# Performance work log

Hardware: AMD Instinct MI355X
Metric: run time of the kernel (lower is better)

## Reference

```python
import jax, jax.numpy as jnp
import numpy as np

NU, NI, ED, H = 30000, 10000, 64, 4
D = ED * H            # fusion_dim = 256
N = NU + NI           # total graph nodes
E = 100000            # edges
B = 8192              # scored (user, wine) pairs
NST, SD = 4, 64       # side tokens / side token dim
NEG = -1e30


def setup_inputs():
    key = jax.random.key(0)
    ks = iter(jax.random.split(key, 64))

    def w(*shape):
        return jax.random.normal(next(ks), shape, jnp.float32) * 0.05

    return {
        "user": jax.random.randint(next(ks), (B,), 0, NU),
        "wine": jax.random.randint(next(ks), (B,), 0, NI),
        "edge_index": jax.random.randint(next(ks), (2, E), 0, N),
        "keep_edge": jax.random.uniform(next(ks), (E,)) > 0.2,   # edge_dropout keep mask
        "node_mask": jax.random.uniform(next(ks), (N,)) < 0.2,   # mask-autoencoding mask
        "user_emb": w(NU, ED),
        "wine_emb": w(NI, ED),
        "up_w": w(ED, D), "up_b": w(D),
        "wp_w": w(ED, D), "wp_b": w(D),
        "sf_proj_w": w(SD, D), "sf_proj_b": w(D),
        "sf_q_w": w(D, D), "sf_q_b": w(D),
        "sf_k_w": w(D, D), "sf_k_b": w(D),
        "sf_v_w": w(D, D), "sf_v_b": w(D),
        "sf_o_w": w(D, D), "sf_o_b": w(D),
        "sf_fc_w": w(2 * D, D), "sf_fc_b": w(D),
        "g_w": w(D, D), "g_b": w(D),
        "t_q_w": w(D, H * D), "t_q_b": w(H * D),
        "t_k_w": w(D, H * D), "t_k_b": w(H * D),
        "t_v_w": w(D, H * D), "t_v_b": w(H * D),
        "t_skip_w": w(D, D), "t_skip_b": w(D),
        "fc_w": w(2 * D, 1), "fc_b": w(1),
        "ae_w": w(D, D), "ae_b": w(D),
        "ep_w": w(2 * D, 1), "ep_b": w(1),
        "wine_side_features": jax.random.normal(next(ks), (NI, NST, SD), jnp.float32),
    }


def _forward(user, wine, edge_index, keep_edge, node_mask,
             user_emb, wine_emb, up_w, up_b, wp_w, wp_b,
             sf_proj_w, sf_proj_b, sf_q_w, sf_q_b, sf_k_w, sf_k_b,
             sf_v_w, sf_v_b, sf_o_w, sf_o_b, sf_fc_w, sf_fc_b,
             g_w, g_b, t_q_w, t_q_b, t_k_w, t_k_b, t_v_w, t_v_b,
             t_skip_w, t_skip_b, fc_w, fc_b, ae_w, ae_b, ep_w, ep_b,
             wine_side_features):
    u_proj = user_emb @ up_w + up_b                       # [NU, D]
    w_proj = wine_emb @ wp_w + wp_b                       # [NI, D]

    # WineSideFusion: single-head attention of wine embedding over side tokens
    side = wine_side_features @ sf_proj_w + sf_proj_b     # [NI, T, D]
    q = w_proj @ sf_q_w + sf_q_b                          # [NI, D]
    k = side @ sf_k_w + sf_k_b                            # [NI, T, D]
    v = side @ sf_v_w + sf_v_b
    attn = jax.nn.softmax(jnp.einsum('nd,ntd->nt', q, k) / jnp.sqrt(jnp.float32(D)), axis=-1)
    ao = jnp.einsum('nt,ntd->nd', attn, v) @ sf_o_w + sf_o_b
    fused = jnp.concatenate([w_proj, ao], axis=1) @ sf_fc_w + sf_fc_b

    x = jnp.concatenate([u_proj, fused], axis=0)          # [N, D]
    src, dst = edge_index[0], edge_index[1]
    ew = keep_edge.astype(x.dtype)                        # edge dropout as 0/1 weights

    # GCNConv (add self loops, symmetric norm)
    deg = jax.ops.segment_sum(ew, dst, num_segments=N) + 1.0
    dinv = jax.lax.rsqrt(deg)
    norm = dinv[src] * dinv[dst] * ew                     # [E]
    xw = x @ g_w                                          # [N, D]
    agg = jax.ops.segment_sum(xw[src] * norm[:, None], dst, num_segments=N)
    x = agg + xw * (dinv * dinv)[:, None] + g_b

    # TransformerConv(heads=H, concat=False): mean over heads + skip
    qh = (x @ t_q_w + t_q_b).reshape(N, H, D)
    kh = (x @ t_k_w + t_k_b).reshape(N, H, D)
    vh = (x @ t_v_w + t_v_b).reshape(N, H, D)
    logits = jnp.einsum('ehd,ehd->eh', qh[dst], kh[src]) / jnp.sqrt(jnp.float32(D))
    logits = jnp.where(keep_edge[:, None], logits, NEG)
    m = jax.ops.segment_max(logits, dst, num_segments=N)  # [N, H]
    m = jnp.where(m < NEG / 2, 0.0, m)                    # guard empty segments
    e = jnp.exp(logits - m[dst]) * ew[:, None]            # [E, H]
    den = jax.ops.segment_sum(e, dst, num_segments=N)     # [N, H]
    num = jax.ops.segment_sum(e[:, :, None] * vh[src], dst, num_segments=N)  # [N, H, D]
    attn_out = num / jnp.maximum(den, 1e-16)[:, :, None]
    x = attn_out.mean(axis=1) + x @ t_skip_w + t_skip_b   # [N, D]

    # Masked autoencoding: masked rows are zeroed, then autoencoded -> recon = bias
    maskf = node_mask.astype(x.dtype)
    recon = ae_b                                          # 0 @ ae_w + ae_b
    diff = recon[None, :] - x                             # [N, D]
    recon_loss = jnp.sum(maskf[:, None] * diff * diff) / (jnp.sum(maskf) * D)

    u_out = x[user]                                       # [B, D]
    w_out = x[wine + NU]                                  # [B, D]
    pair = jnp.concatenate([u_out, w_out], axis=1)        # [B, 2D]

    edge_score = jax.nn.sigmoid(pair @ ep_w + ep_b)       # [B, 1]
    edge_pred_loss = jnp.mean((edge_score - 1.0) ** 2)

    score = jax.nn.sigmoid((pair @ fc_w + fc_b).squeeze(-1)) * 4.0 + 1.0  # [B]
    return score, recon_loss, edge_pred_loss


def reference(user, wine, edge_index, keep_edge, node_mask,
              user_emb, wine_emb, up_w, up_b, wp_w, wp_b,
              sf_proj_w, sf_proj_b, sf_q_w, sf_q_b, sf_k_w, sf_k_b,
              sf_v_w, sf_v_b, sf_o_w, sf_o_b, sf_fc_w, sf_fc_b,
              g_w, g_b, t_q_w, t_q_b, t_k_w, t_k_b, t_v_w, t_v_b,
              t_skip_w, t_skip_b, fc_w, fc_b, ae_w, ae_b, ep_w, ep_b,
              wine_side_features):
    return _forward(user, wine, edge_index, keep_edge, node_mask,
                    user_emb, wine_emb, up_w, up_b, wp_w, wp_b,
                    sf_proj_w, sf_proj_b, sf_q_w, sf_q_b, sf_k_w, sf_k_b,
                    sf_v_w, sf_v_b, sf_o_w, sf_o_b, sf_fc_w, sf_fc_b,
                    g_w, g_b, t_q_w, t_q_b, t_k_w, t_k_b, t_v_w, t_v_b,
                    t_skip_w, t_skip_b, fc_w, fc_b, ae_w, ae_b, ep_w, ep_b,
                    wine_side_features)
```

## Files before the change

### kernel.cpp

```cpp
#include <hip/hip_runtime.h>
#include <stdint.h>

typedef unsigned short u16;
typedef unsigned char u8;
typedef __attribute__((ext_vector_type(8))) short bf16x8;
typedef __attribute__((ext_vector_type(4))) float f32x4;

#define NU_C 30000
#define NI_C 10000
#define N_C  40000
#define E_C  100000
#define B_C  8192

static __device__ __forceinline__ float bf2f(u16 u) {
    union { unsigned int i; float f; } c; c.i = ((unsigned int)u) << 16; return c.f;
}
static __device__ __forceinline__ u16 f2bf(float f) {
    union { float f; unsigned int i; } c; c.f = f;
    return (u16)((c.i + 0x7FFFu + ((c.i >> 16) & 1u)) >> 16);
}
static __device__ __forceinline__ float wave_sum(float v) {
#pragma unroll
    for (int off = 32; off > 0; off >>= 1) v += __shfl_xor(v, off);
    return v;
}
static __device__ __forceinline__ float group_sum16(float v) {
#pragma unroll
    for (int off = 8; off > 0; off >>= 1) v += __shfl_xor(v, off);
    return v;
}
static __device__ __forceinline__ float dot16(const bf16x8 a0, const bf16x8 a1,
                                              const bf16x8 b0, const bf16x8 b1) {
    float p = 0.f;
#pragma unroll
    for (int j = 0; j < 8; ++j) p = fmaf(bf2f((u16)a0[j]), bf2f((u16)b0[j]), p);
#pragma unroll
    for (int j = 0; j < 8; ++j) p = fmaf(bf2f((u16)a1[j]), bf2f((u16)b1[j]), p);
    return p;
}

__global__ void zero_kernel(unsigned int* p, int n) {
    int i = blockIdx.x * 256 + threadIdx.x;
    if (i < n) p[i] = 0u;
}
__global__ void fillval_kernel(float* p, int n, float v) {
    int i = blockIdx.x * 256 + threadIdx.x;
    if (i < n) p[i] = v;
}

__global__ void detect_kernel(const unsigned int* a, int n, int* flag) {
    int i = blockIdx.x * 256 + threadIdx.x;
    if (i >= n) return;
    unsigned int v = a[i];
    int f = 0;
    if (v > 1u) f |= 1;
    if (v != 0u && v != 0x3F800000u) f |= 2;
    if (f) atomicOr(flag, f);
}
__global__ void conv_masks_kernel(const void* keep_raw, const void* nm_raw,
                                  u8* km, u8* nm, int E, int N, const int* flag)
{
    int i = blockIdx.x * 256 + threadIdx.x;
    const int f = *flag;
    if (i < E) {
        u8 r;
        if ((f & 1) == 0)      r = ((const int*)keep_raw)[i] != 0;
        else if ((f & 2) == 0) r = ((const float*)keep_raw)[i] != 0.f;
        else                   r = ((const u8*)keep_raw)[i] != 0;
        km[i] = r;
    }
    int j = i - E;
    if (j >= 0 && j < N) {
        u8 r;
        if ((f & 1) == 0)      r = ((const int*)nm_raw)[j] != 0;
        else if ((f & 2) == 0) r = ((const float*)nm_raw)[j] != 0.f;
        else                   r = ((const u8*)nm_raw)[j] != 0;
        nm[j] = r;
    }
}

__global__ void conv3_kernel(const float* __restrict__ a, int na4,
                             const float* __restrict__ b, int nb4,
                             const float* __restrict__ c, int nc4,
                             u16* __restrict__ oa, u16* __restrict__ ob, u16* __restrict__ oc)
{
    int tot = na4 + nb4 + nc4;
    for (int i = blockIdx.x * 256 + threadIdx.x; i < tot; i += gridDim.x * 256) {
        const float* s; u16* o; int j = i;
        if (j < na4) { s = a; o = oa; }
        else if ((j -= na4) < nb4) { s = b; o = ob; }
        else { j -= nb4; s = c; o = oc; }
        float4 v = *(const float4*)&s[(size_t)j * 4];
        ushort4 r;
        r.x = f2bf(v.x); r.y = f2bf(v.y); r.z = f2bf(v.z); r.w = f2bf(v.w);
        *(ushort4*)&o[(size_t)j * 4] = r;
    }
}

#define WT_ELEMS 1359872
__device__ const int wd_prefix[23] = {0,16384,32768,49152,114688,180224,245760,311296,442368,
    507904,573440,638976,704512,770048,835584,901120,966656,1032192,1097728,1163264,1228800,
    1294336,1359872};
__device__ const u8  wd_src[22]  = {0,1,2,3,4,5,6,7,8,9,10,11,12,10,11,12,10,11,12,10,11,12};
__device__ const short wd_ldw[22]= {256,256,256,256,256,256,256,256,256,256,
    1024,1024,1024,1024,1024,1024,1024,1024,1024,1024,1024,1024};
__device__ const short wd_coff[22]={0,0,0,0,0,0,0,0,0,0, 0,0,0, 256,256,256, 512,512,512, 768,768,768};
__device__ const short wd_kmask[22]={63,63,63,255,255,255,255,511,255,255,
    255,255,255,255,255,255,255,255,255,255,255,255};
__device__ const u8  wd_ksh[22] = {6,6,6,8,8,8,8,9,8,8, 8,8,8,8,8,8,8,8,8,8,8,8};

__global__ __launch_bounds__(256)
void wtrans_kernel(const float* w0, const float* w1, const float* w2, const float* w3,
                   const float* w4, const float* w5, const float* w6, const float* w7,
                   const float* w8, const float* w9, const float* w10, const float* w11,
                   const float* w12, u16* __restrict__ WT)
{
    int idx = blockIdx.x * 256 + threadIdx.x;
    if (idx >= WT_ELEMS) return;
    int d = 0;
    while (wd_prefix[d + 1] <= idx) ++d;
    const int local = idx - wd_prefix[d];
    const int k = local & wd_kmask[d];
    const int n = local >> wd_ksh[d];
    const float* s;
    switch (wd_src[d]) {
        case 0: s = w0; break; case 1: s = w1; break; case 2: s = w2; break;
        case 3: s = w3; break; case 4: s = w4; break; case 5: s = w5; break;
        case 6: s = w6; break; case 7: s = w7; break; case 8: s = w8; break;
        case 9: s = w9; break; case 10: s = w10; break; case 11: s = w11; break;
        default: s = w12; break;
    }
    WT[idx] = f2bf(s[(size_t)k * wd_ldw[d] + wd_coff[d] + n]);
}

__global__ void prep_bias_kernel(const float* sfk_b, const float* sfv_b,
                                 const float* tq_b, const float* tk_b, const float* tv_b,
                                 float* kvb, float* qkvb)
{
    int i = blockIdx.x * 256 + threadIdx.x;
    if (i < 512) kvb[i] = i < 256 ? sfk_b[i] : sfv_b[i - 256];
    if (i < 3072) {
        int h = i / 768, j = i - h * 768;
        qkvb[i] = j < 256 ? tq_b[h * 256 + j]
                : (j < 512 ? tk_b[h * 256 + j - 256] : tv_b[h * 256 + j - 512]);
    }
}

template <typename OT>
__global__ __launch_bounds__(512)
void mgemm_kernel(const u16* __restrict__ A, int lda,
                  const u16* __restrict__ WT,
                  const float* __restrict__ bias,
                  OT* __restrict__ C, int ldc,
                  int M, int N, int K)
{
    __shared__ __align__(16) u16 As[256][72];
    __shared__ __align__(16) u16 Bs[128][72];
    const int t = threadIdx.x;
    const int wid = t >> 6, lane = t & 63;
    const int wr = wid >> 1, wc = wid & 1;
    const int lr = lane & 15, lg = lane >> 4;
    const int gx = gridDim.x;
    const int nwg = gx * gridDim.y;
    const int orig = blockIdx.y * gx + blockIdx.x;
    const int q8 = nwg >> 3, r8 = nwg & 7;
    const int xcd = orig & 7, oidx = orig >> 3;
    const int swzb = (xcd < r8 ? xcd * (q8 + 1) : r8 * (q8 + 1) + (xcd - r8) * q8) + oidx;
    const int row0 = (swzb / gx) * 256, col0 = (swzb % gx) * 128;
    const int sra = t >> 1, sha = (t & 1) * 32;
    const int srb = t >> 2, shb = (t & 3) * 16;
    const bool avalid = (row0 + sra) < M;
    const u16* aptr = &A[(size_t)min(row0 + sra, M - 1) * lda];
    const u16* bptr = &WT[(size_t)(col0 + srb) * K];
    const bf16x8 z = {0, 0, 0, 0, 0, 0, 0, 0};
    f32x4 acc[4][4] = {};
    bf16x8 ra[4], rb[2];

    auto gload = [&](int k0) {
#pragma unroll
        for (int j = 0; j < 4; ++j)
            ra[j] = avalid ? *(const bf16x8*)&aptr[k0 + sha + j * 8] : z;
#pragma unroll
        for (int j = 0; j < 2; ++j)
            rb[j] = *(const bf16x8*)&bptr[k0 + shb + j * 8];
    };
    auto swrite = [&]() {
#pragma unroll
        for (int j = 0; j < 4; ++j)
            *(bf16x8*)&As[sra][sha + j * 8] = ra[j];
#pragma unroll
        for (int j = 0; j < 2; ++j)
            *(bf16x8*)&Bs[srb][shb + j * 8] = rb[j];
    };
    auto compute = [&]() {
#pragma unroll
        for (int kk = 0; kk < 2; ++kk) {
            bf16x8 af[4], bfr[4];
#pragma unroll
            for (int m = 0; m < 4; ++m)
                af[m] = *(const bf16x8*)&As[wr * 64 + m * 16 + lr][kk * 32 + lg * 8];
#pragma unroll
            for (int n = 0; n < 4; ++n)
                bfr[n] = *(const bf16x8*)&Bs[wc * 64 + n * 16 + lr][kk * 32 + lg * 8];
#pragma unroll
            for (int m = 0; m < 4; ++m)
#pragma unroll
                for (int n = 0; n < 4; ++n)
                    acc[m][n] = __builtin_amdgcn_mfma_f32_16x16x32_bf16(af[m], bfr[n], acc[m][n], 0, 0, 0);
        }
    };

    gload(0);
    swrite();
    __syncthreads();
    for (int k0 = 64; k0 < K; k0 += 64) {
        gload(k0);
        compute();
        __syncthreads();
        swrite();
        __syncthreads();
    }
    compute();

#pragma unroll
    for (int m = 0; m < 4; ++m) {
#pragma unroll
        for (int r = 0; r < 4; ++r) {
            int row = row0 + wr * 64 + m * 16 + lg * 4 + r;
            if (row >= M) continue;
#pragma unroll
            for (int n = 0; n < 4; ++n) {
                int col = col0 + wc * 64 + n * 16 + lr;
                float v = acc[m][n][r];
                if (bias) v += bias[col];
                if constexpr (sizeof(OT) == 4) C[(size_t)row * ldc + col] = v;
                else C[(size_t)row * ldc + col] = f2bf(v);
            }
        }
    }
}

__global__ __launch_bounds__(256)
void side_attn_kernel(const u16* __restrict__ q, const u16* __restrict__ kv,
                      u16* __restrict__ ao, int NI)
{
    const int wid = threadIdx.x >> 6, lane = threadIdx.x & 63;
    const int n = blockIdx.x * 4 + wid;
    if (n >= NI) return;
    const ushort4 qu = *(const ushort4*)&q[(size_t)n * 256 + lane * 4];
    const float q0 = bf2f(qu.x), q1 = bf2f(qu.y), q2 = bf2f(qu.z), q3 = bf2f(qu.w);
    float logit[4];
#pragma unroll
    for (int tk = 0; tk < 4; ++tk) {
        const ushort4 ku = *(const ushort4*)&kv[((size_t)n * 4 + tk) * 512 + lane * 4];
        float p = q0 * bf2f(ku.x) + q1 * bf2f(ku.y) + q2 * bf2f(ku.z) + q3 * bf2f(ku.w);
        logit[tk] = wave_sum(p) * (1.f / 16.f);
    }
    float mx = fmaxf(fmaxf(logit[0], logit[1]), fmaxf(logit[2], logit[3]));
    float e[4], den = 0.f;
#pragma unroll
    for (int tk = 0; tk < 4; ++tk) { e[tk] = __expf(logit[tk] - mx); den += e[tk]; }
    const float inv = 1.f / den;
    float o0 = 0.f, o1 = 0.f, o2 = 0.f, o3 = 0.f;
#pragma unroll
    for (int tk = 0; tk < 4; ++tk) {
        const ushort4 vu = *(const ushort4*)&kv[((size_t)n * 4 + tk) * 512 + 256 + lane * 4];
        const float w = e[tk] * inv;
        o0 = fmaf(w, bf2f(vu.x), o0); o1 = fmaf(w, bf2f(vu.y), o1);
        o2 = fmaf(w, bf2f(vu.z), o2); o3 = fmaf(w, bf2f(vu.w), o3);
    }
    ushort4 o;
    o.x = f2bf(o0); o.y = f2bf(o1); o.z = f2bf(o2); o.w = f2bf(o3);
    *(ushort4*)&ao[(size_t)n * 256 + lane * 4] = o;
}

__global__ void count_kernel(const int* __restrict__ dst, const u8* __restrict__ keep,
                             int* __restrict__ cnt, float* __restrict__ degw, int E)
{
    int e = blockIdx.x * 256 + threadIdx.x;
    if (e >= E) return;
    int d = dst[e];
    atomicAdd(&cnt[d], 1);
    if (keep[e]) atomicAdd(&degw[d], 1.f);
}

__global__ void dinv_kernel(const float* __restrict__ degw, float* __restrict__ dinv, int N)
{
    int n = blockIdx.x * 256 + threadIdx.x;
    if (n < N) dinv[n] = rsqrtf(degw[n] + 1.f);
}

__global__ __launch_bounds__(1024)
void scan_kernel(const int* __restrict__ cnt, int* __restrict__ rs, int n)
{
    __shared__ int wsum[17];
    __shared__ int s_run;
    const int t = threadIdx.x, lane = t & 63, wid = t >> 6;
    if (t == 0) s_run = 0;
    __syncthreads();
    for (int base = 0; base < n; base += 1024) {
        int i = base + t;
        int v = (i < n) ? cnt[i] : 0;
        int x = v;
#pragma unroll
        for (int off = 1; off < 64; off <<= 1) {
            int y = __shfl_up(x, off);
            if (lane >= off) x += y;
        }
        if (lane == 63) wsum[wid] = x;
        __syncthreads();
        if (t == 0) {
            int a = 0;
            for (int j = 0; j < 16; ++j) { int tmp = wsum[j]; wsum[j] = a; a += tmp; }
            wsum[16] = a;
        }
        __syncthreads();
        if (i < n) rs[i] = s_run + wsum[wid] + x - v;
        __syncthreads();
        if (t == 0) s_run += wsum[16];
        __syncthreads();
    }
    if (t == 0) rs[n] = s_run;
}

__global__ void fill_kernel(const int* __restrict__ dst, const int* __restrict__ rs,
                            int* __restrict__ cursor, int* __restrict__ eid, int E)
{
    int e = blockIdx.x * 256 + threadIdx.x;
    if (e >= E) return;
    int d = dst[e];
    int p = atomicAdd(&cursor[d], 1);
    eid[rs[d] + p] = e;
}

__global__ void sort_kernel(const int* __restrict__ rs, int* __restrict__ eid, int N)
{
    int n = blockIdx.x * 256 + threadIdx.x;
    if (n >= N) return;
    const int b = rs[n], len = rs[n + 1] - b;
    for (int i = 1; i < len; ++i) {
        int key = eid[b + i];
        int j = i - 1;
        while (j >= 0 && eid[b + j] > key) { eid[b + j + 1] = eid[b + j]; --j; }
        eid[b + j + 1] = key;
    }
}

__global__ void edge_prep_kernel(const int* __restrict__ eid, const int* __restrict__ src,
                                 const int* __restrict__ dst, const u8* __restrict__ keep,
                                 const float* __restrict__ dinv,
                                 int* __restrict__ ssrc, float* __restrict__ wnorm, int E)
{
    int i = blockIdx.x * 256 + threadIdx.x;
    if (i >= E) return;
    const int e = eid[i];
    const int s = src[e];
    const u8 k = keep[e];
    ssrc[i] = s * 2 + (int)k;
    wnorm[i] = k ? dinv[s] * dinv[dst[e]] : 0.f;
}

__global__ __launch_bounds__(256)
void gcn_kernel(const u16* __restrict__ xw, const int* __restrict__ ssrc,
                const float* __restrict__ wnorm, const int* __restrict__ rs,
                const float* __restrict__ dinv, const float* __restrict__ gb,
                u16* __restrict__ xout, int N)
{
    const int wid = threadIdx.x >> 6, lane = threadIdx.x & 63;
    const int n = blockIdx.x * 4 + wid;
    if (n >= N) return;
    const float di = dinv[n];
    const float dii = di * di;
    const ushort4 own = *(const ushort4*)&xw[(size_t)n * 256 + lane * 4];
    float a0 = bf2f(own.x) * dii, a1 = bf2f(own.y) * dii;
    float a2 = bf2f(own.z) * dii, a3 = bf2f(own.w) * dii;
    const int e0 = rs[n], e1 = rs[n + 1];
    int i = e0;
    for (; i + 1 < e1; i += 2) {
        const float wa = wnorm[i], wb = wnorm[i + 1];
        const int sa = ssrc[i] >> 1, sb = ssrc[i + 1] >> 1;
        const ushort4 ra = *(const ushort4*)&xw[(size_t)sa * 256 + lane * 4];
        const ushort4 rb = *(const ushort4*)&xw[(size_t)sb * 256 + lane * 4];
        a0 = fmaf(bf2f(rb.x), wb, fmaf(bf2f(ra.x), wa, a0));
        a1 = fmaf(bf2f(rb.y), wb, fmaf(bf2f(ra.y), wa, a1));
        a2 = fmaf(bf2f(rb.z), wb, fmaf(bf2f(ra.z), wa, a2));
        a3 = fmaf(bf2f(rb.w), wb, fmaf(bf2f(ra.w), wa, a3));
    }
    if (i < e1) {
        const float wa = wnorm[i];
        const int sa = ssrc[i] >> 1;
        const ushort4 r = *(const ushort4*)&xw[(size_t)sa * 256 + lane * 4];
        a0 = fmaf(bf2f(r.x), wa, a0); a1 = fmaf(bf2f(r.y), wa, a1);
        a2 = fmaf(bf2f(r.z), wa, a2); a3 = fmaf(bf2f(r.w), wa, a3);
    }
    const float4 g = *(const float4*)&gb[lane * 4];
    ushort4 o;
    o.x = f2bf(a0 + g.x); o.y = f2bf(a1 + g.y);
    o.z = f2bf(a2 + g.z); o.w = f2bf(a3 + g.w);
    *(ushort4*)&xout[(size_t)n * 256 + lane * 4] = o;
}

__global__ __launch_bounds__(256)
void tconv_all_kernel(const u16* __restrict__ qkv, const int* __restrict__ ssrc,
                      const int* __restrict__ rs, float* __restrict__ xacc, int N)
{
    const int wid = threadIdx.x >> 6, lane = threadIdx.x & 63;
    const int g = lane >> 4, s = lane & 15;
    const int n = blockIdx.x * 16 + wid * 4 + g;
    if (n >= N) return;
    const int e0 = rs[n], e1 = rs[n + 1];
    float fin[16] = {};
    for (int h = 0; h < 4; ++h) {
        const size_t qb0 = (size_t)n * 3072 + h * 768;
        const bf16x8 qa = *(const bf16x8*)&qkv[qb0 + s * 16];
        const bf16x8 qb = *(const bf16x8*)&qkv[qb0 + s * 16 + 8];
        float m = -1e30f, den = 0.f;
        float ac[16] = {};
        int i = e0;
        for (; i + 1 < e1; i += 2) {
            const int va = ssrc[i], vb = ssrc[i + 1];
            const size_t sa = (size_t)(va >> 1) * 3072 + h * 768;
            const size_t sb = (size_t)(vb >> 1) * 3072 + h * 768;
            const float ewa = (float)(va & 1), ewb = (float)(vb & 1);
            const bf16x8 ka0 = *(const bf16x8*)&qkv[sa + 256 + s * 16];
            const bf16x8 ka1 = *(const bf16x8*)&qkv[sa + 256 + s * 16 + 8];
            const bf16x8 kb0 = *(const bf16x8*)&qkv[sb + 256 + s * 16];
            const bf16x8 kb1 = *(const bf16x8*)&qkv[sb + 256 + s * 16 + 8];
            const bf16x8 xa0 = *(const bf16x8*)&qkv[sa + 512 + s * 16];
            const bf16x8 xa1 = *(const bf16x8*)&qkv[sa + 512 + s * 16 + 8];
            const bf16x8 xb0 = *(const bf16x8*)&qkv[sb + 512 + s * 16];
            const bf16x8 xb1 = *(const bf16x8*)&qkv[sb + 512 + s * 16 + 8];
            float pa = group_sum16(dot16(qa, qb, ka0, ka1)) * (1.f / 16.f);
            float pb = group_sum16(dot16(qa, qb, kb0, kb1)) * (1.f / 16.f);
            {
                const float mn = fmaxf(m, pa);
                const float sc = __expf(m - mn);
                const float w = __expf(pa - mn) * ewa;
                den = den * sc + w;
#pragma unroll
                for (int j = 0; j < 8; ++j) ac[j] = fmaf(w, bf2f((u16)xa0[j]), ac[j] * sc);
#pragma unroll
                for (int j = 0; j < 8; ++j) ac[8 + j] = fmaf(w, bf2f((u16)xa1[j]), ac[8 + j] * sc);
                m = mn;
            }
            {
                const float mn = fmaxf(m, pb);
                const float sc = __expf(m - mn);
                const float w = __expf(pb - mn) * ewb;
                den = den * sc + w;
#pragma unroll
                for (int j = 0; j < 8; ++j) ac[j] = fmaf(w, bf2f((u16)xb0[j]), ac[j] * sc);
#pragma unroll
                for (int j = 0; j < 8; ++j) ac[8 + j] = fmaf(w, bf2f((u16)xb1[j]), ac[8 + j] * sc);
                m = mn;
            }
        }
        if (i < e1) {
            const int va = ssrc[i];
            const size_t sa = (size_t)(va >> 1) * 3072 + h * 768;
            const float ewa = (float)(va & 1);
            const bf16x8 ka0 = *(const bf16x8*)&qkv[sa + 256 + s * 16];
            const bf16x8 ka1 = *(const bf16x8*)&qkv[sa + 256 + s * 16 + 8];
            const bf16x8 xa0 = *(const bf16x8*)&qkv[sa + 512 + s * 16];
            const bf16x8 xa1 = *(const bf16x8*)&qkv[sa + 512 + s * 16 + 8];
            float pa = group_sum16(dot16(qa, qb, ka0, ka1)) * (1.f / 16.f);
            const float mn = fmaxf(m, pa);
            const float sc = __expf(m - mn);
            const float w = __expf(pa - mn) * ewa;
            den = den * sc + w;
#pragma unroll
            for (int j = 0; j < 8; ++j) ac[j] = fmaf(w, bf2f((u16)xa0[j]), ac[j] * sc);
#pragma unroll
            for (int j = 0; j < 8; ++j) ac[8 + j] = fmaf(w, bf2f((u16)xa1[j]), ac[8 + j] * sc);
        }
        const float inv = 0.25f / fmaxf(den, 1e-16f);
#pragma unroll
        for (int j = 0; j < 16; ++j) fin[j] += ac[j] * inv;
    }
    float4* p4 = (float4*)&xacc[(size_t)n * 256 + s * 16];
#pragma unroll
    for (int q = 0; q < 4; ++q) {
        float4 cur = p4[q];
        cur.x += fin[q * 4 + 0]; cur.y += fin[q * 4 + 1];
        cur.z += fin[q * 4 + 2]; cur.w += fin[q * 4 + 3];
        p4[q] = cur;
    }
}

__global__ __launch_bounds__(256)
void tconv_head_kernel(const u16* __restrict__ qkv, const int* __restrict__ ssrc,
                       const int* __restrict__ rs, float* __restrict__ xacc, int N)
{
    const int wid = threadIdx.x >> 6, lane = threadIdx.x & 63;
    const int g = lane >> 4, s = lane & 15;
    const int n = blockIdx.x * 16 + wid * 4 + g;
    if (n >= N) return;
    const bf16x8 qa = *(const bf16x8*)&qkv[(size_t)n * 768 + s * 16];
    const bf16x8 qb = *(const bf16x8*)&qkv[(size_t)n * 768 + s * 16 + 8];
    const int e0 = rs[n], e1 = rs[n + 1];
    float m = -1e30f, den = 0.f;
    float ac[16] = {};
    int i = e0;
    for (; i + 1 < e1; i += 2) {
        const int va = ssrc[i], vb = ssrc[i + 1];
        const size_t sa = (size_t)(va >> 1) * 768, sb = (size_t)(vb >> 1) * 768;
        const float ewa = (float)(va & 1), ewb = (float)(vb & 1);
        const bf16x8 ka0 = *(const bf16x8*)&qkv[sa + 256 + s * 16];
        const bf16x8 ka1 = *(const bf16x8*)&qkv[sa + 256 + s * 16 + 8];
        const bf16x8 kb0 = *(const bf16x8*)&qkv[sb + 256 + s * 16];
        const bf16x8 kb1 = *(const bf16x8*)&qkv[sb + 256 + s * 16 + 8];
        const bf16x8 xa0 = *(const bf16x8*)&qkv[sa + 512 + s * 16];
        const bf16x8 xa1 = *(const bf16x8*)&qkv[sa + 512 + s * 16 + 8];
        const bf16x8 xb0 = *(const bf16x8*)&qkv[sb + 512 + s * 16];
        const bf16x8 xb1 = *(const bf16x8*)&qkv[sb + 512 + s * 16 + 8];
        float pa = group_sum16(dot16(qa, qb, ka0, ka1)) * (1.f / 16.f);
        float pb = group_sum16(dot16(qa, qb, kb0, kb1)) * (1.f / 16.f);
        {
            const float mn = fmaxf(m, pa);
            const float sc = __expf(m - mn);
            const float w = __expf(pa - mn) * ewa;
            den = den * sc + w;
#pragma unroll
            for (int j = 0; j < 8; ++j) ac[j] = fmaf(w, bf2f((u16)xa0[j]), ac[j] * sc);
#pragma unroll
            for (int j = 0; j < 8; ++j) ac[8 + j] = fmaf(w, bf2f((u16)xa1[j]), ac[8 + j] * sc);
            m = mn;
        }
        {
            const float mn = fmaxf(m, pb);
            const float sc = __expf(m - mn);
            const float w = __expf(pb - mn) * ewb;
            den = den * sc + w;
#pragma unroll
            for (int j = 0; j < 8; ++j) ac[j] = fmaf(w, bf2f((u16)xb0[j]), ac[j] * sc);
#pragma unroll
            for (int j = 0; j < 8; ++j) ac[8 + j] = fmaf(w, bf2f((u16)xb1[j]), ac[8 + j] * sc);
            m = mn;
        }
    }
    if (i < e1) {
        const int va = ssrc[i];
        const size_t sa = (size_t)(va >> 1) * 768;
        const float ewa = (float)(va & 1);
        const bf16x8 ka0 = *(const bf16x8*)&qkv[sa + 256 + s * 16];
        const bf16x8 ka1 = *(const bf16x8*)&qkv[sa + 256 + s * 16 + 8];
        const bf16x8 xa0 = *(const bf16x8*)&qkv[sa + 512 + s * 16];
        const bf16x8 xa1 = *(const bf16x8*)&qkv[sa + 512 + s * 16 + 8];
        float pa = group_sum16(dot16(qa, qb, ka0, ka1)) * (1.f / 16.f);
        const float mn = fmaxf(m, pa);
        const float sc = __expf(m - mn);
        const float w = __expf(pa - mn) * ewa;
        den = den * sc + w;
#pragma unroll
        for (int j = 0; j < 8; ++j) ac[j] = fmaf(w, bf2f((u16)xa0[j]), ac[j] * sc);
#pragma unroll
        for (int j = 0; j < 8; ++j) ac[8 + j] = fmaf(w, bf2f((u16)xa1[j]), ac[8 + j] * sc);
    }
    const float inv = 0.25f / fmaxf(den, 1e-16f);
    float4* p4 = (float4*)&xacc[(size_t)n * 256 + s * 16];
#pragma unroll
    for (int q = 0; q < 4; ++q) {
        float4 cur = p4[q];
        cur.x += ac[q * 4 + 0] * inv; cur.y += ac[q * 4 + 1] * inv;
        cur.z += ac[q * 4 + 2] * inv; cur.w += ac[q * 4 + 3] * inv;
        p4[q] = cur;
    }
}

__global__ __launch_bounds__(256)
void recon_kernel(const float* __restrict__ x, const u8* __restrict__ mask,
                  const float* __restrict__ aeb,
                  float* __restrict__ rblkS, float* __restrict__ rblkC, int N)
{
    const int total = N * 256;
    float s = 0.f, c = 0.f;
    for (int idx = blockIdx.x * 256 + threadIdx.x; idx < total; idx += gridDim.x * 256) {
        const int n = idx >> 8, d = idx & 255;
        if (mask[n]) {
            const float diff = aeb[d] - x[idx];
            s = fmaf(diff, diff, s);
            if (d == 0) c += 1.f;
        }
    }
    s = wave_sum(s); c = wave_sum(c);
    __shared__ float ss[4], cc[4];
    const int lane = threadIdx.x & 63, wid = threadIdx.x >> 6;
    if (lane == 0) { ss[wid] = s; cc[wid] = c; }
    __syncthreads();
    if (threadIdx.x == 0) {
        rblkS[blockIdx.x] = ss[0] + ss[1] + ss[2] + ss[3];
        rblkC[blockIdx.x] = cc[0] + cc[1] + cc[2] + cc[3];
    }
}

__global__ __launch_bounds__(256)
void score_kernel(const float* __restrict__ x, const int* __restrict__ user,
                  const int* __restrict__ wine,
                  const float* __restrict__ epw, const float* __restrict__ epb,
                  const float* __restrict__ fcw, const float* __restrict__ fcb,
                  float* __restrict__ out, float* __restrict__ sblk, int B)
{
    __shared__ float sep[4];
    const int wid = threadIdx.x >> 6, lane = threadIdx.x & 63;
    const int b = blockIdx.x * 4 + wid;
    if (b < B) {
        const size_t u = (size_t)user[b];
        const size_t w = (size_t)wine[b] + NU_C;
        const float4 xu = *(const float4*)&x[u * 256 + lane * 4];
        const float4 xw = *(const float4*)&x[w * 256 + lane * 4];
        const float4 e1 = *(const float4*)&epw[lane * 4];
        const float4 e2 = *(const float4*)&epw[256 + lane * 4];
        const float4 f1 = *(const float4*)&fcw[lane * 4];
        const float4 f2 = *(const float4*)&fcw[256 + lane * 4];
        float pep = xu.x * e1.x + xu.y * e1.y + xu.z * e1.z + xu.w * e1.w
                  + xw.x * e2.x + xw.y * e2.y + xw.z * e2.z + xw.w * e2.w;
        float pfc = xu.x * f1.x + xu.y * f1.y + xu.z * f1.z + xu.w * f1.w
                  + xw.x * f2.x + xw.y * f2.y + xw.z * f2.z + xw.w * f2.w;
        pep = wave_sum(pep); pfc = wave_sum(pfc);
        if (lane == 0) {
            const float es = 1.f / (1.f + __expf(-(pep + epb[0])));
            sep[wid] = (es - 1.f) * (es - 1.f);
            out[b] = 1.f / (1.f + __expf(-(pfc + fcb[0]))) * 4.f + 1.f;
        }
    } else if (lane == 0) {
        sep[wid] = 0.f;
    }
    __syncthreads();
    if (threadIdx.x == 0) sblk[blockIdx.x] = sep[0] + sep[1] + sep[2] + sep[3];
}

__global__ __launch_bounds__(1024)
void final_reduce_kernel(const float* __restrict__ rblkS, const float* __restrict__ rblkC,
                         const float* __restrict__ sblk, float* __restrict__ out, int B)
{
    const int t = threadIdx.x, lane = t & 63, wid = t >> 6;
    float s = rblkS[t] + rblkS[t + 1024];
    float c = rblkC[t] + rblkC[t + 1024];
    float p = sblk[t] + sblk[t + 1024];
    s = wave_sum(s); c = wave_sum(c); p = wave_sum(p);
    __shared__ float ss[16], cc[16], pp[16];
    if (lane == 0) { ss[wid] = s; cc[wid] = c; pp[wid] = p; }
    __syncthreads();
    if (t == 0) {
        float S = 0.f, C = 0.f, P = 0.f;
        for (int i = 0; i < 16; ++i) { S += ss[i]; C += cc[i]; P += pp[i]; }
        out[B] = S / (C * 256.f);
        out[B + 1] = P / (float)B;
    }
}

extern "C" void kernel_launch(void* const* d_in, const int* in_sizes, int n_in,
                              void* d_out, int out_size, void* d_ws, size_t ws_size,
                              hipStream_t stream)
{
    const int* user = (const int*)d_in[0];
    const int* wine = (const int*)d_in[1];
    const int* e_src = (const int*)d_in[2];
    const int* e_dst = e_src + E_C;
    const void* keep_raw  = d_in[3];
    const void* nmask_raw = d_in[4];
    const float* user_emb = (const float*)d_in[5];
    const float* wine_emb = (const float*)d_in[6];
    const float* up_w = (const float*)d_in[7];
    const float* up_b = (const float*)d_in[8];
    const float* wp_w = (const float*)d_in[9];
    const float* wp_b = (const float*)d_in[10];
    const float* sf_proj_w = (const float*)d_in[11];
    const float* sf_proj_b = (const float*)d_in[12];
    const float* sf_q_w = (const float*)d_in[13];
    const float* sf_q_b = (const float*)d_in[14];
    const float* sf_k_w = (const float*)d_in[15];
    const float* sf_k_b = (const float*)d_in[16];
    const float* sf_v_w = (const float*)d_in[17];
    const float* sf_v_b = (const float*)d_in[18];
    const float* sf_o_w = (const float*)d_in[19];
    const float* sf_o_b = (const float*)d_in[20];
    const float* sf_fc_w = (const float*)d_in[21];
    const float* sf_fc_b = (const float*)d_in[22];
    const float* g_w = (const float*)d_in[23];
    const float* g_b = (const float*)d_in[24];
    const float* t_q_w = (const float*)d_in[25];
    const float* t_q_b = (const float*)d_in[26];
    const float* t_k_w = (const float*)d_in[27];
    const float* t_k_b = (const float*)d_in[28];
    const float* t_v_w = (const float*)d_in[29];
    const float* t_v_b = (const float*)d_in[30];
    const float* t_skip_w = (const float*)d_in[31];
    const float* t_skip_b = (const float*)d_in[32];
    const float* fc_w = (const float*)d_in[33];
    const float* fc_b = (const float*)d_in[34];
    const float* ae_b = (const float*)d_in[36];
    const float* ep_w = (const float*)d_in[37];
    const float* ep_b = (const float*)d_in[38];
    const float* wsf = (const float*)d_in[39];
    float* out = (float*)d_out;
    char* ws = (char*)d_ws;

    size_t off = 0;
    auto take = [&](size_t b) { size_t r = off; off += (b + 255) & ~(size_t)255; return r; };
    const size_t o_xb     = take((size_t)N_C * 256 * 2);
    const size_t o_cnt    = take((size_t)N_C * 4);
    const size_t o_degw   = take((size_t)N_C * 4);
    const size_t o_cursor = take((size_t)N_C * 4);
    const size_t o_scal   = take(256);
    const size_t o_rowst  = take((size_t)(N_C + 1) * 4);
    const size_t o_dinv   = take((size_t)N_C * 4);
    const size_t o_eid    = take((size_t)E_C * 4);
    const size_t o_ssrc   = take((size_t)E_C * 4);
    const size_t o_wnorm  = take((size_t)E_C * 4);
    const size_t o_kmask  = take((size_t)E_C);
    const size_t o_nmask  = take((size_t)N_C);
    const size_t o_rblkS  = take(2048 * 4);
    const size_t o_rblkC  = take(2048 * 4);
    const size_t o_sblk   = take(2048 * 4);
    const size_t o_wt     = take((size_t)WT_ELEMS * 2);
    const size_t o_bias   = take(3584 * 4);
    const size_t ARENA_SMALL = 102400000;
    const size_t ARENA_BIG   = 286720000;
    const size_t o_arena  = take(ARENA_SMALL);
    const size_t NEED = off;
    const size_t NEED_BIG = NEED - ARENA_SMALL + ARENA_BIG;
    const bool big = ws_size >= NEED_BIG;

    if (ws_size < NEED) {
        fillval_kernel<<<dim3((out_size + 255) / 256), 256, 0, stream>>>(
            out, out_size, (float)((double)ws_size / (1024.0 * 1024.0)));
        return;
    }

    u16*   xb     = (u16*)  (ws + o_xb);
    int*   cnt    = (int*)  (ws + o_cnt);
    float* degw   = (float*)(ws + o_degw);
    int*   cursor = (int*)  (ws + o_cursor);
    int*   flag   = (int*)  (ws + o_scal);
    int*   rowst  = (int*)  (ws + o_rowst);
    float* dinvb  = (float*)(ws + o_dinv);
    int*   eid    = (int*)  (ws + o_eid);
    int*   ssrc   = (int*)  (ws + o_ssrc);
    float* wnorm  = (float*)(ws + o_wnorm);
    u8*    kmask  = (u8*)   (ws + o_kmask);
    u8*    nmaskb = (u8*)   (ws + o_nmask);
    float* rblkS  = (float*)(ws + o_rblkS);
    float* rblkC  = (float*)(ws + o_rblkC);
    float* sblk   = (float*)(ws + o_sblk);
    u16*   WT     = (u16*)  (ws + o_wt);
    float* kvb    = (float*)(ws + o_bias);
    float* qkvb   = kvb + 512;

    u16* wt_up   = WT + 0;
    u16* wt_wp   = WT + 16384;
    u16* wt_proj = WT + 32768;
    u16* wt_sfq  = WT + 49152;
    u16* wt_sfkv = WT + 114688;
    u16* wt_sfo  = WT + 245760;
    u16* wt_sffc = WT + 311296;
    u16* wt_g    = WT + 442368;
    u16* wt_skip = WT + 507904;
    u16* wt_qkv  = WT + 573440;

    u16* ue16  = (u16*)(ws + o_arena);
    u16* we16  = (u16*)(ws + o_arena + 3840000);
    u16* wsf16 = (u16*)(ws + o_arena + 5120000);
    u16* cat   = (u16*)(ws + o_arena + 10240000);
    u16* side  = (u16*)(ws + o_arena + 20480000);
    u16* qbuf  = (u16*)(ws + o_arena + 40960000);
    u16* kvbuf = (u16*)(ws + o_arena + 46080000);
    u16* aobuf = (u16*)(ws + o_arena + 87040000);
    u16* xw    = (u16*)(ws + o_arena);
    u16* qkvh  = (u16*)(ws + o_arena);
    float* xacc_s = (float*)(ws + o_arena + 61440000);
    u16* qkv4  = (u16*)(ws + o_arena);
    float* xacc_b = (float*)(ws + o_arena + 245760000);
    float* xacc = big ? xacc_b : xacc_s;

    const int zero_words = (3 * N_C * 4 + 256) / 4;
    zero_kernel<<<dim3((zero_words + 255) / 256), 256, 0, stream>>>((unsigned int*)cnt, zero_words);

    detect_kernel<<<dim3((E_C / 4 + 255) / 256), 256, 0, stream>>>((const unsigned int*)keep_raw, E_C / 4, flag);
    conv_masks_kernel<<<dim3((E_C + N_C + 255) / 256), 256, 0, stream>>>(keep_raw, nmask_raw, kmask, nmaskb, E_C, N_C, flag);

    conv3_kernel<<<dim3(2048), 256, 0, stream>>>(user_emb, NU_C * 16, wine_emb, NI_C * 16,
                                                 wsf, N_C * 16, ue16, we16, wsf16);
    wtrans_kernel<<<dim3(WT_ELEMS / 256), 256, 0, stream>>>(up_w, wp_w, sf_proj_w, sf_q_w,
        sf_k_w, sf_v_w, sf_o_w, sf_fc_w, g_w, t_skip_w, t_q_w, t_k_w, t_v_w, WT);
    prep_bias_kernel<<<dim3(12), 256, 0, stream>>>(sf_k_b, sf_v_b, t_q_b, t_k_b, t_v_b, kvb, qkvb);

    mgemm_kernel<u16><<<dim3(2, 118), 512, 0, stream>>>(ue16, 64, wt_up, up_b, xb, 256, NU_C, 256, 64);
    mgemm_kernel<u16><<<dim3(2, 40), 512, 0, stream>>>(we16, 64, wt_wp, wp_b, cat, 512, NI_C, 256, 64);
    mgemm_kernel<u16><<<dim3(2, 157), 512, 0, stream>>>(wsf16, 64, wt_proj, sf_proj_b, side, 256, N_C, 256, 64);
    mgemm_kernel<u16><<<dim3(2, 40), 512, 0, stream>>>(cat, 512, wt_sfq, sf_q_b, qbuf, 256, NI_C, 256, 256);
    mgemm_kernel<u16><<<dim3(4, 157), 512, 0, stream>>>(side, 256, wt_sfkv, kvb, kvbuf, 512, N_C, 512, 256);
    side_attn_kernel<<<dim3(2500), 256, 0, stream>>>(qbuf, kvbuf, aobuf, NI_C);
    mgemm_kernel<u16><<<dim3(2, 40), 512, 0, stream>>>(aobuf, 256, wt_sfo, sf_o_b, cat + 256, 512, NI_C, 256, 256);
    mgemm_kernel<u16><<<dim3(2, 40), 512, 0, stream>>>(cat, 512, wt_sffc, sf_fc_b, xb + (size_t)NU_C * 256, 256, NI_C, 256, 512);

    count_kernel<<<dim3((E_C + 255) / 256), 256, 0, stream>>>(e_dst, kmask, cnt, degw, E_C);
    dinv_kernel<<<dim3((N_C + 255) / 256), 256, 0, stream>>>(degw, dinvb, N_C);
    scan_kernel<<<dim3(1), 1024, 0, stream>>>(cnt, rowst, N_C);
    fill_kernel<<<dim3((E_C + 255) / 256), 256, 0, stream>>>(e_dst, rowst, cursor, eid, E_C);
    sort_kernel<<<dim3((N_C + 255) / 256), 256, 0, stream>>>(rowst, eid, N_C);
    edge_prep_kernel<<<dim3((E_C + 255) / 256), 256, 0, stream>>>(eid, e_src, e_dst, kmask, dinvb, ssrc, wnorm, E_C);

    mgemm_kernel<u16><<<dim3(2, 157), 512, 0, stream>>>(xb, 256, wt_g, nullptr, xw, 256, N_C, 256, 256);
    gcn_kernel<<<dim3(N_C / 4), 256, 0, stream>>>(xw, ssrc, wnorm, rowst, dinvb, g_b, xb, N_C);

    mgemm_kernel<float><<<dim3(2, 157), 512, 0, stream>>>(xb, 256, wt_skip, t_skip_b, xacc, 256, N_C, 256, 256);
    if (big) {
        mgemm_kernel<u16><<<dim3(24, 157), 512, 0, stream>>>(xb, 256, wt_qkv, qkvb, qkv4, 3072, N_C, 3072, 256);
        tconv_all_kernel<<<dim3(N_C / 16), 256, 0, stream>>>(qkv4, ssrc, rowst, xacc, N_C);
    } else {
        for (int h = 0; h < 4; ++h) {
            mgemm_kernel<u16><<<dim3(6, 157), 512, 0, stream>>>(xb, 256, wt_qkv + h * 196608,
                                                                qkvb + h * 768, qkvh, 768, N_C, 768, 256);
            tconv_head_kernel<<<dim3(N_C / 16), 256, 0, stream>>>(qkvh, ssrc, rowst, xacc, N_C);
        }
    }

    recon_kernel<<<dim3(2048), 256, 0, stream>>>(xacc, nmaskb, ae_b, rblkS, rblkC, N_C);
    score_kernel<<<dim3(2048), 256, 0, stream>>>(xacc, user, wine, ep_w, ep_b, fc_w, fc_b, out, sblk, B_C);
    final_reduce_kernel<<<dim3(1), 1024, 0, stream>>>(rblkS, rblkC, sblk, out, B_C);
}
```

Measured before the change: 610.0 us.

## Pre-tile weights into MFMA fragment layout and load B directly from global

```diff
diff --git a/kernel.cpp b/kernel.cpp
--- a/kernel.cpp
+++ b/kernel.cpp
@@ -95,6 +95,14 @@
         r.x = f2bf(v.x); r.y = f2bf(v.y); r.z = f2bf(v.z); r.w = f2bf(v.w);
         *(ushort4*)&o[(size_t)j * 4] = r;
     }
+}
+
+static __device__ __forceinline__ int tiled_idx(int n, int k, int K) {
+    return (n >> 6) * ((K >> 5) << 11)
+         + (k >> 5) * 2048
+         + ((n >> 4) & 3) * 512
+         + ((((k >> 3) & 3) * 16 + (n & 15)) << 3)
+         + (k & 7);
 }
 
 #define WT_ELEMS 1359872
@@ -122,6 +130,7 @@
     const int local = idx - wd_prefix[d];
     const int k = local & wd_kmask[d];
     const int n = local >> wd_ksh[d];
+    const int K = (int)wd_kmask[d] + 1;
     const float* s;
     switch (wd_src[d]) {
         case 0: s = w0; break; case 1: s = w1; break; case 2: s = w2; break;
@@ -130,7 +139,7 @@
         case 9: s = w9; break; case 10: s = w10; break; case 11: s = w11; break;
         default: s = w12; break;
     }
-    WT[idx] = f2bf(s[(size_t)k * wd_ldw[d] + wd_coff[d] + n]);
+    WT[wd_prefix[d] + tiled_idx(n, k, K)] = f2bf(s[(size_t)k * wd_ldw[d] + wd_coff[d] + n]);
 }
 
 __global__ void prep_bias_kernel(const float* sfk_b, const float* sfv_b,
@@ -155,7 +164,6 @@
                   int M, int N, int K)
 {
     __shared__ __align__(16) u16 As[256][72];
-    __shared__ __align__(16) u16 Bs[128][72];
     const int t = threadIdx.x;
     const int wid = t >> 6, lane = t & 63;
     const int wr = wid >> 1, wc = wid & 1;
@@ -168,40 +176,34 @@
     const int swzb = (xcd < r8 ? xcd * (q8 + 1) : r8 * (q8 + 1) + (xcd - r8) * q8) + oidx;
     const int row0 = (swzb / gx) * 256, col0 = (swzb % gx) * 128;
     const int sra = t >> 1, sha = (t & 1) * 32;
-    const int srb = t >> 2, shb = (t & 3) * 16;
     const bool avalid = (row0 + sra) < M;
     const u16* aptr = &A[(size_t)min(row0 + sra, M - 1) * lda];
-    const u16* bptr = &WT[(size_t)(col0 + srb) * K];
+    const u16* bft = WT + (size_t)((col0 >> 6) + wc) * ((K >> 5) << 11) + lane * 8;
     const bf16x8 z = {0, 0, 0, 0, 0, 0, 0, 0};
     f32x4 acc[4][4] = {};
-    bf16x8 ra[4], rb[2];
+    bf16x8 ra[4];
 
     auto gload = [&](int k0) {
 #pragma unroll
         for (int j = 0; j < 4; ++j)
             ra[j] = avalid ? *(const bf16x8*)&aptr[k0 + sha + j * 8] : z;
-#pragma unroll
-        for (int j = 0; j < 2; ++j)
-            rb[j] = *(const bf16x8*)&bptr[k0 + shb + j * 8];
     };
     auto swrite = [&]() {
 #pragma unroll
         for (int j = 0; j < 4; ++j)
             *(bf16x8*)&As[sra][sha + j * 8] = ra[j];
-#pragma unroll
-        for (int j = 0; j < 2; ++j)
-            *(bf16x8*)&Bs[srb][shb + j * 8] = rb[j];
     };
-    auto compute = [&]() {
+    auto compute = [&](int kb) {
 #pragma unroll
         for (int kk = 0; kk < 2; ++kk) {
             bf16x8 af[4], bfr[4];
+            const u16* bp2 = bft + (size_t)(kb + kk) * 2048;
+#pragma unroll
+            for (int n = 0; n < 4; ++n)
+                bfr[n] = *(const bf16x8*)&bp2[n * 512];
 #pragma unroll
             for (int m = 0; m < 4; ++m)
                 af[m] = *(const bf16x8*)&As[wr * 64 + m * 16 + lr][kk * 32 + lg * 8];
-#pragma unroll
-            for (int n = 0; n < 4; ++n)
-                bfr[n] = *(const bf16x8*)&Bs[wc * 64 + n * 16 + lr][kk * 32 + lg * 8];
 #pragma unroll
             for (int m = 0; m < 4; ++m)
 #pragma unroll
@@ -213,14 +215,16 @@
     gload(0);
     swrite();
     __syncthreads();
+    int kb = 0;
     for (int k0 = 64; k0 < K; k0 += 64) {
         gload(k0);
-        compute();
+        compute(kb);
         __syncthreads();
         swrite();
         __syncthreads();
-    }
-    compute();
+        kb += 2;
+    }
+    compute(kb);
 
 #pragma unroll
     for (int m = 0; m < 4; ++m) {
```

After: 734.1 us. 1.2x slower.
